# Optimization experiments

Measured on AMD Instinct MI355X. Metric: run time of the kernel, lower is better.

Reference implementation:

```python
import jax, jax.numpy as jnp
import numpy as np

B, H, S, D = 2, 16, 2048, 128


def setup_inputs() -> dict:
    key = jax.random.key(0)
    kq, kk, kv, km = jax.random.split(key, 4)
    Q = jax.random.normal(kq, (B, H, S, D), dtype=jnp.float32)
    K = jax.random.normal(kk, (B, H, S, D), dtype=jnp.float32)
    V = jax.random.normal(kv, (B, H, S, D), dtype=jnp.float32)
    mask = jax.random.randint(km, (B, 1, S, S), 0, 2, dtype=jnp.int32)
    scale = jnp.float32(1.0 / np.sqrt(D))
    return {"Q": Q, "K": K, "V": V, "mask": mask, "scale": scale}


def reference(Q, K, V, mask, scale):
    # attention scores: [B, H, Sq, Sk]
    attention = jnp.einsum('bhqd,bhkd->bhqk', Q, K) * scale
    NEG_BIG = jnp.float32(-1e9)
    attention = jnp.where(mask == 0, NEG_BIG, attention)
    attention = jax.nn.softmax(attention, axis=-1)
    # context: [B, H, Sq, Dv]
    context = jnp.einsum('bhqk,bhkd->bhqd', attention, V)
    return (context, attention)
```

## Files before the change

### kernel.cpp

```cpp
#include <hip/hip_runtime.h>

#define Bb 2
#define Hh 16
#define Ss 2048
#define Dd 128
#define NWrd (Ss / 64)

typedef _Float16 half_t;
typedef __attribute__((ext_vector_type(4))) float floatx4;
typedef __attribute__((ext_vector_type(8))) _Float16 halfx8;
typedef unsigned long long u64;

__global__ __launch_bounds__(256) void cvt_qk_kernel(
    const float* __restrict__ Q, const float* __restrict__ K,
    const float* __restrict__ scale_p,
    half_t* __restrict__ Qh, half_t* __restrict__ Kh) {
  const float s = scale_p[0];
  size_t i = ((size_t)blockIdx.x * 256 + threadIdx.x) * 8;
  floatx4 a0 = *(const floatx4*)(Q + i);
  floatx4 a1 = *(const floatx4*)(Q + i + 4);
  halfx8 hq = {(half_t)(a0.x * s), (half_t)(a0.y * s), (half_t)(a0.z * s),
               (half_t)(a0.w * s), (half_t)(a1.x * s), (half_t)(a1.y * s),
               (half_t)(a1.z * s), (half_t)(a1.w * s)};
  *(halfx8*)(Qh + i) = hq;
  floatx4 b0 = *(const floatx4*)(K + i);
  floatx4 b1 = *(const floatx4*)(K + i + 4);
  halfx8 hk = {(half_t)b0.x, (half_t)b0.y, (half_t)b0.z, (half_t)b0.w,
               (half_t)b1.x, (half_t)b1.y, (half_t)b1.z, (half_t)b1.w};
  *(halfx8*)(Kh + i) = hk;
}

__global__ __launch_bounds__(256) void vt_kernel(const float* __restrict__ V,
                                                 half_t* __restrict__ Vt) {
  __shared__ __align__(16) half_t t[64 * 72];
  const int bh = blockIdx.z;
  const int k0 = blockIdx.x * 64;
  const int d0 = blockIdx.y * 64;
  const int tid = threadIdx.x;
  const float* src = V + ((size_t)bh * Ss + k0) * Dd + d0;
  for (int idx = tid; idx < 64 * 16; idx += 256) {
    int r = idx >> 4;
    int c4 = (idx & 15) << 2;
    floatx4 v = *(const floatx4*)(src + (size_t)r * Dd + c4);
    t[(c4 + 0) * 72 + r] = (half_t)v.x;
    t[(c4 + 1) * 72 + r] = (half_t)v.y;
    t[(c4 + 2) * 72 + r] = (half_t)v.z;
    t[(c4 + 3) * 72 + r] = (half_t)v.w;
  }
  __syncthreads();
  half_t* dst = Vt + ((size_t)bh * Dd + d0) * Ss + k0;
  for (int idx = tid; idx < 64 * 8; idx += 256) {
    int r = idx >> 3;
    int c8 = (idx & 7) << 3;
    *(halfx8*)(dst + (size_t)r * Ss + c8) = *(const halfx8*)&t[r * 72 + c8];
  }
}

__global__ __launch_bounds__(256) void mask_pack_kernel(
    const int* __restrict__ mask, u64* __restrict__ mb) {
  size_t w = (size_t)blockIdx.x * 4 + (threadIdx.x >> 6);
  int lane = threadIdx.x & 63;
  int m = mask[w * 64 + lane];
  u64 bal = __ballot(m != 0);
  if (lane == 0) mb[w] = bal;
}

__global__ __launch_bounds__(256) void attn_kernel(
    const half_t* __restrict__ Qh, const half_t* __restrict__ Kh,
    const u64* __restrict__ Mb, const half_t* __restrict__ Vt,
    float* __restrict__ ctx_out, float* __restrict__ attn_out) {
  __shared__ __align__(16) half_t Ks[64 * 136];
  __shared__ __align__(16) half_t Vts[128 * 72];
  __shared__ __align__(16) half_t Ps[4 * 16 * 72];

  const int tid = threadIdx.x;
  const int wave = tid >> 6;
  const int lane = tid & 63;
  const int quad = lane >> 4;
  const int l16 = lane & 15;
  const int q0 = blockIdx.x * 64;
  const int bh = blockIdx.z * Hh + blockIdx.y;

  const half_t* Qg = Qh + ((size_t)bh * Ss + q0) * Dd;
  const half_t* Kg = Kh + (size_t)bh * Ss * Dd;
  const half_t* Vtg = Vt + (size_t)bh * Dd * Ss;
  const u64* Mg = Mb + ((size_t)blockIdx.z * Ss + q0) * NWrd;

  for (int it = 0; it < 4; ++it) {
    int idx = tid + it * 256;
    int r = idx >> 4, c8 = (idx & 15) << 3;
    *(halfx8*)&Ks[r * 136 + c8] = *(const halfx8*)(Qg + (size_t)r * Dd + c8);
  }
  __syncthreads();
  const int arow = 16 * wave + l16;
  halfx8 qa[4];
#pragma unroll
  for (int ks = 0; ks < 4; ++ks)
    qa[ks] = *(const halfx8*)&Ks[arow * 136 + ks * 32 + quad * 8];

  const int lrow = 16 * wave + quad * 4;
  const int qrow = q0 + lrow;
  float lacc[4] = {0.f, 0.f, 0.f, 0.f};

  for (int kt = 0; kt < NWrd; ++kt) {
    const int k0 = kt * 64;
    __syncthreads();
    for (int it = 0; it < 4; ++it) {
      int idx = tid + it * 256;
      int r = idx >> 4, c8 = (idx & 15) << 3;
      *(halfx8*)&Ks[r * 136 + c8] = *(const halfx8*)(Kg + (size_t)(k0 + r) * Dd + c8);
    }
    u64 mw[4];
#pragma unroll
    for (int r = 0; r < 4; ++r) mw[r] = Mg[(size_t)(lrow + r) * NWrd + kt];
    __syncthreads();
#pragma unroll
    for (int nt = 0; nt < 4; ++nt) {
      floatx4 acc = {0.f, 0.f, 0.f, 0.f};
#pragma unroll
      for (int ks = 0; ks < 4; ++ks) {
        halfx8 bf = *(const halfx8*)&Ks[(nt * 16 + l16) * 136 + ks * 32 + quad * 8];
        acc = __builtin_amdgcn_mfma_f32_16x16x32_f16(qa[ks], bf, acc, 0, 0, 0);
      }
      const int sh = nt * 16 + l16;
#pragma unroll
      for (int r = 0; r < 4; ++r) {
        float e = ((mw[r] >> sh) & 1) ? __expf(acc[r]) : 0.0f;
        lacc[r] += e;
      }
    }
  }
  float inv[4];
#pragma unroll
  for (int r = 0; r < 4; ++r) {
    float s = lacc[r];
    s += __shfl_xor(s, 1);
    s += __shfl_xor(s, 2);
    s += __shfl_xor(s, 4);
    s += __shfl_xor(s, 8);
    inv[r] = 1.0f / s;
  }

  floatx4 cacc[8];
#pragma unroll
  for (int i = 0; i < 8; ++i) cacc[i] = (floatx4){0.f, 0.f, 0.f, 0.f};
  float* attn_base = attn_out + (size_t)bh * Ss * Ss;

  for (int kt = 0; kt < NWrd; ++kt) {
    const int k0 = kt * 64;
    __syncthreads();
    for (int it = 0; it < 4; ++it) {
      int idx = tid + it * 256;
      int r = idx >> 4, c8 = (idx & 15) << 3;
      *(halfx8*)&Ks[r * 136 + c8] = *(const halfx8*)(Kg + (size_t)(k0 + r) * Dd + c8);
    }
    for (int it = 0; it < 4; ++it) {
      int idx = tid + it * 256;
      int r = idx >> 3, c8 = (idx & 7) << 3;
      *(halfx8*)&Vts[r * 72 + c8] = *(const halfx8*)(Vtg + (size_t)r * Ss + k0 + c8);
    }
    u64 mw[4];
#pragma unroll
    for (int r = 0; r < 4; ++r) mw[r] = Mg[(size_t)(lrow + r) * NWrd + kt];
    __syncthreads();
#pragma unroll
    for (int nt = 0; nt < 4; ++nt) {
      floatx4 acc = {0.f, 0.f, 0.f, 0.f};
#pragma unroll
      for (int ks = 0; ks < 4; ++ks) {
        halfx8 bf = *(const halfx8*)&Ks[(nt * 16 + l16) * 136 + ks * 32 + quad * 8];
        acc = __builtin_amdgcn_mfma_f32_16x16x32_f16(qa[ks], bf, acc, 0, 0, 0);
      }
      const int sh = nt * 16 + l16;
#pragma unroll
      for (int r = 0; r < 4; ++r) {
        float p = ((mw[r] >> sh) & 1) ? __expf(acc[r]) * inv[r] : 0.0f;
        __builtin_nontemporal_store(p, &attn_base[(size_t)(qrow + r) * Ss + k0 + sh]);
        Ps[wave * (16 * 72) + (quad * 4 + r) * 72 + sh] = (half_t)p;
      }
    }
    halfx8 pa[2];
    pa[0] = *(const halfx8*)&Ps[wave * (16 * 72) + l16 * 72 + quad * 8];
    pa[1] = *(const halfx8*)&Ps[wave * (16 * 72) + l16 * 72 + 32 + quad * 8];
#pragma unroll
    for (int nt2 = 0; nt2 < 8; ++nt2) {
#pragma unroll
      for (int ks = 0; ks < 2; ++ks) {
        halfx8 bv = *(const halfx8*)&Vts[(nt2 * 16 + l16) * 72 + ks * 32 + quad * 8];
        cacc[nt2] = __builtin_amdgcn_mfma_f32_16x16x32_f16(pa[ks], bv, cacc[nt2], 0, 0, 0);
      }
    }
  }

  float* ctx = ctx_out + (size_t)bh * Ss * Dd;
#pragma unroll
  for (int nt2 = 0; nt2 < 8; ++nt2) {
#pragma unroll
    for (int r = 0; r < 4; ++r) {
      ctx[(size_t)(qrow + r) * Dd + nt2 * 16 + l16] = cacc[nt2][r];
    }
  }
}

extern "C" void kernel_launch(void* const* d_in, const int* in_sizes, int n_in,
                              void* d_out, int out_size, void* d_ws, size_t ws_size,
                              hipStream_t stream) {
  const float* Q = (const float*)d_in[0];
  const float* K = (const float*)d_in[1];
  const float* V = (const float*)d_in[2];
  const int* mask = (const int*)d_in[3];
  const float* scale = (const float*)d_in[4];
  float* ctx = (float*)d_out;
  float* attn = (float*)d_out + (size_t)Bb * Hh * Ss * Dd;

  const size_t nqk = (size_t)Bb * Hh * Ss * Dd;
  half_t* Qh = (half_t*)d_ws;
  half_t* Kh = Qh + nqk;
  half_t* Vt = Kh + nqk;
  u64* Mbits = (u64*)(Vt + nqk);

  cvt_qk_kernel<<<nqk / (256 * 8), 256, 0, stream>>>(Q, K, scale, Qh, Kh);
  dim3 gt(Ss / 64, Dd / 64, Bb * Hh);
  vt_kernel<<<gt, 256, 0, stream>>>(V, Vt);
  mask_pack_kernel<<<((size_t)Bb * Ss * NWrd) / 4, 256, 0, stream>>>(mask, Mbits);
  dim3 gm(Ss / 64, Hh, Bb);
  attn_kernel<<<gm, 256, 0, stream>>>(Qh, Kh, Mbits, Vt, ctx, attn);
}
```

Before: 941.8 us.

## Prefetch K tiles into registers, read V directly from global, remap blocks

Loads of the next K tile now go into registers while the current tile is computed, so global latency overlaps the MFMA work. The V shared-memory staging is removed: each lane fetches its V^T fragments straight from global/L2 for the PV MFMAs. Q fragments are also read directly from global. Block indices are swizzled so that consecutive workgroups spread across heads, and launch bounds request 4 blocks per CU. The intent is lower LDS use and less load latency, at the cost of more register pressure and uncoalesced, repeated global V reads across the waves.

```diff
diff --git a/kernel.cpp b/kernel.cpp
--- a/kernel.cpp
+++ b/kernel.cpp
@@ -5,6 +5,7 @@
 #define Ss 2048
 #define Dd 128
 #define NWrd (Ss / 64)
+#define NBLK (Bb * Hh * (Ss / 64))
 
 typedef _Float16 half_t;
 typedef __attribute__((ext_vector_type(4))) float floatx4;
@@ -65,12 +66,11 @@
   if (lane == 0) mb[w] = bal;
 }
 
-__global__ __launch_bounds__(256) void attn_kernel(
+__global__ __launch_bounds__(256, 4) void attn_kernel(
     const half_t* __restrict__ Qh, const half_t* __restrict__ Kh,
     const u64* __restrict__ Mb, const half_t* __restrict__ Vt,
     float* __restrict__ ctx_out, float* __restrict__ attn_out) {
   __shared__ __align__(16) half_t Ks[64 * 136];
-  __shared__ __align__(16) half_t Vts[128 * 72];
   __shared__ __align__(16) half_t Ps[4 * 16 * 72];
 
   const int tid = threadIdx.x;
@@ -78,41 +78,51 @@
   const int lane = tid & 63;
   const int quad = lane >> 4;
   const int l16 = lane & 15;
-  const int q0 = blockIdx.x * 64;
-  const int bh = blockIdx.z * Hh + blockIdx.y;
+
+  const int wg = blockIdx.x + 32 * (blockIdx.y + Hh * blockIdx.z);
+  const int v = (wg & 7) * (NBLK / 8) + (wg >> 3);
+  const int q0 = (v & 31) * 64;
+  const int bh = v >> 5;
+  const int bidx = bh >> 4;
 
   const half_t* Qg = Qh + ((size_t)bh * Ss + q0) * Dd;
   const half_t* Kg = Kh + (size_t)bh * Ss * Dd;
   const half_t* Vtg = Vt + (size_t)bh * Dd * Ss;
-  const u64* Mg = Mb + ((size_t)blockIdx.z * Ss + q0) * NWrd;
-
-  for (int it = 0; it < 4; ++it) {
-    int idx = tid + it * 256;
-    int r = idx >> 4, c8 = (idx & 15) << 3;
-    *(halfx8*)&Ks[r * 136 + c8] = *(const halfx8*)(Qg + (size_t)r * Dd + c8);
-  }
-  __syncthreads();
+  const u64* Mg = Mb + ((size_t)bidx * Ss + q0) * NWrd;
+
   const int arow = 16 * wave + l16;
   halfx8 qa[4];
 #pragma unroll
   for (int ks = 0; ks < 4; ++ks)
-    qa[ks] = *(const halfx8*)&Ks[arow * 136 + ks * 32 + quad * 8];
+    qa[ks] = *(const halfx8*)(Qg + (size_t)arow * Dd + ks * 32 + quad * 8);
 
   const int lrow = 16 * wave + quad * 4;
   const int qrow = q0 + lrow;
+  const u64* Mrow = Mg + (size_t)lrow * NWrd;
   float lacc[4] = {0.f, 0.f, 0.f, 0.f};
+
+  const int s_r = tid >> 4;
+  const int s_c = (tid & 15) << 3;
+
+  halfx8 kpre[4];
+#pragma unroll
+  for (int it = 0; it < 4; ++it)
+    kpre[it] = *(const halfx8*)(Kg + (size_t)(s_r + it * 16) * Dd + s_c);
 
   for (int kt = 0; kt < NWrd; ++kt) {
     const int k0 = kt * 64;
     __syncthreads();
-    for (int it = 0; it < 4; ++it) {
-      int idx = tid + it * 256;
-      int r = idx >> 4, c8 = (idx & 15) << 3;
-      *(halfx8*)&Ks[r * 136 + c8] = *(const halfx8*)(Kg + (size_t)(k0 + r) * Dd + c8);
+#pragma unroll
+    for (int it = 0; it < 4; ++it)
+      *(halfx8*)&Ks[(s_r + it * 16) * 136 + s_c] = kpre[it];
+    if (kt + 1 < NWrd) {
+#pragma unroll
+      for (int it = 0; it < 4; ++it)
+        kpre[it] = *(const halfx8*)(Kg + (size_t)(k0 + 64 + s_r + it * 16) * Dd + s_c);
     }
     u64 mw[4];
 #pragma unroll
-    for (int r = 0; r < 4; ++r) mw[r] = Mg[(size_t)(lrow + r) * NWrd + kt];
+    for (int r = 0; r < 4; ++r) mw[r] = Mrow[(size_t)r * NWrd + kt];
     __syncthreads();
 #pragma unroll
     for (int nt = 0; nt < 4; ++nt) {
@@ -144,24 +154,26 @@
   floatx4 cacc[8];
 #pragma unroll
   for (int i = 0; i < 8; ++i) cacc[i] = (floatx4){0.f, 0.f, 0.f, 0.f};
-  float* attn_base = attn_out + (size_t)bh * Ss * Ss;
+  float* attn_row = attn_out + (size_t)bh * Ss * Ss + (size_t)qrow * Ss;
+
+#pragma unroll
+  for (int it = 0; it < 4; ++it)
+    kpre[it] = *(const halfx8*)(Kg + (size_t)(s_r + it * 16) * Dd + s_c);
 
   for (int kt = 0; kt < NWrd; ++kt) {
     const int k0 = kt * 64;
     __syncthreads();
-    for (int it = 0; it < 4; ++it) {
-      int idx = tid + it * 256;
-      int r = idx >> 4, c8 = (idx & 15) << 3;
-      *(halfx8*)&Ks[r * 136 + c8] = *(const halfx8*)(Kg + (size_t)(k0 + r) * Dd + c8);
-    }
-    for (int it = 0; it < 4; ++it) {
-      int idx = tid + it * 256;
-      int r = idx >> 3, c8 = (idx & 7) << 3;
-      *(halfx8*)&Vts[r * 72 + c8] = *(const halfx8*)(Vtg + (size_t)r * Ss + k0 + c8);
+#pragma unroll
+    for (int it = 0; it < 4; ++it)
+      *(halfx8*)&Ks[(s_r + it * 16) * 136 + s_c] = kpre[it];
+    if (kt + 1 < NWrd) {
+#pragma unroll
+      for (int it = 0; it < 4; ++it)
+        kpre[it] = *(const halfx8*)(Kg + (size_t)(k0 + 64 + s_r + it * 16) * Dd + s_c);
     }
     u64 mw[4];
 #pragma unroll
-    for (int r = 0; r < 4; ++r) mw[r] = Mg[(size_t)(lrow + r) * NWrd + kt];
+    for (int r = 0; r < 4; ++r) mw[r] = Mrow[(size_t)r * NWrd + kt];
     __syncthreads();
 #pragma unroll
     for (int nt = 0; nt < 4; ++nt) {
@@ -175,20 +187,19 @@
 #pragma unroll
       for (int r = 0; r < 4; ++r) {
         float p = ((mw[r] >> sh) & 1) ? __expf(acc[r]) * inv[r] : 0.0f;
-        __builtin_nontemporal_store(p, &attn_base[(size_t)(qrow + r) * Ss + k0 + sh]);
+        __builtin_nontemporal_store(p, &attn_row[(size_t)r * Ss + k0 + sh]);
         Ps[wave * (16 * 72) + (quad * 4 + r) * 72 + sh] = (half_t)p;
       }
     }
-    halfx8 pa[2];
-    pa[0] = *(const halfx8*)&Ps[wave * (16 * 72) + l16 * 72 + quad * 8];
-    pa[1] = *(const halfx8*)&Ps[wave * (16 * 72) + l16 * 72 + 32 + quad * 8];
+    halfx8 pa0 = *(const halfx8*)&Ps[wave * (16 * 72) + l16 * 72 + quad * 8];
+    halfx8 pa1 = *(const halfx8*)&Ps[wave * (16 * 72) + l16 * 72 + 32 + quad * 8];
 #pragma unroll
     for (int nt2 = 0; nt2 < 8; ++nt2) {
-#pragma unroll
-      for (int ks = 0; ks < 2; ++ks) {
-        halfx8 bv = *(const halfx8*)&Vts[(nt2 * 16 + l16) * 72 + ks * 32 + quad * 8];
-        cacc[nt2] = __builtin_amdgcn_mfma_f32_16x16x32_f16(pa[ks], bv, cacc[nt2], 0, 0, 0);
-      }
+      const half_t* vrow = Vtg + (size_t)(nt2 * 16 + l16) * Ss + k0 + quad * 8;
+      halfx8 bv0 = *(const halfx8*)(vrow);
+      cacc[nt2] = __builtin_amdgcn_mfma_f32_16x16x32_f16(pa0, bv0, cacc[nt2], 0, 0, 0);
+      halfx8 bv1 = *(const halfx8*)(vrow + 32);
+      cacc[nt2] = __builtin_amdgcn_mfma_f32_16x16x32_f16(pa1, bv1, cacc[nt2], 0, 0, 0);
     }
   }
 
```

Result: faster. 887.2 us (-5.8%).
